# Optimization experiments

Measured on AMD Instinct MI355X. Metric: run time of the kernel, lower is better.

## Reference

```python
import jax, jax.numpy as jnp
import numpy as np

B, L, ENC, DEC, ATT = 128, 196, 2048, 512, 512

def setup_inputs() -> dict:
    key = jax.random.key(0)
    ks = jax.random.split(key, 8)
    s_enc = 1.0 / np.sqrt(ENC)
    s_dec = 1.0 / np.sqrt(DEC)
    s_att = 1.0 / np.sqrt(ATT)
    return {
        "encoder_out": jax.random.normal(ks[0], (B, L, ENC), jnp.float32),
        "decoder_hidden": jax.random.normal(ks[1], (B, DEC), jnp.float32),
        "We": jax.random.uniform(ks[2], (ENC, ATT), jnp.float32, -s_enc, s_enc),
        "be": jax.random.uniform(ks[3], (ATT,), jnp.float32, -s_enc, s_enc),
        "Wd": jax.random.uniform(ks[4], (DEC, ATT), jnp.float32, -s_dec, s_dec),
        "bd": jax.random.uniform(ks[5], (ATT,), jnp.float32, -s_dec, s_dec),
        "wa": jax.random.uniform(ks[6], (ATT,), jnp.float32, -s_att, s_att),
        "ba": jax.random.uniform(ks[7], (), jnp.float32, -s_att, s_att),
    }

def reference(encoder_out, decoder_hidden, We, be, Wd, bd, wa, ba):
    # encoder_out: [B, L, ENC]; decoder_hidden: [B, DEC]
    enc_map = jnp.einsum('ble,ea->bla', encoder_out, We) + be          # [B, L, A]
    dec_map = decoder_hidden @ Wd + bd                                  # [B, A]
    scores = jnp.tanh(enc_map + dec_map[:, None, :]) @ wa + ba         # [B, L]
    alphas = jax.nn.softmax(scores, axis=1)                             # [B, L]
    context = jnp.einsum('bl,ble->be', alphas, encoder_out)             # [B, ENC]
    return (context, alphas)
```

## Files before the change

kernel.cpp:

```cpp
#include <hip/hip_runtime.h>

#define B_   128
#define L_   196
#define ENC_ 2048
#define DEC_ 512
#define ATT_ 512
#define M_   (B_ * L_)

typedef _Float16 f16x4 __attribute__((ext_vector_type(4)));
typedef _Float16 f16x8 __attribute__((ext_vector_type(8)));
typedef __fp16   h16x2 __attribute__((ext_vector_type(2)));
typedef float    f32x4 __attribute__((ext_vector_type(4)));

#define FENCE_LDS_BARRIER()                                        \
    do {                                                           \
        asm volatile("s_waitcnt lgkmcnt(0)" ::: "memory");         \
        __builtin_amdgcn_s_barrier();                              \
        __builtin_amdgcn_sched_barrier(0);                         \
    } while (0)


__global__ void wets_kernel(const float* __restrict__ We, _Float16* __restrict__ WeTs) {
    int u = blockIdx.x * 256 + threadIdx.x;
    int row = u & 127;
    int k8  = (u >> 7) & 3;
    int kt  = (u >> 9) & 63;
    int nt  = u >> 15;
    int n  = nt * 128 + row;
    int k0 = kt * 32 + k8 * 8;
    f16x8 h;
#pragma unroll
    for (int j = 0; j < 8; ++j) h[j] = (_Float16)We[(k0 + j) * ATT_ + n];
    *reinterpret_cast<f16x8*>(WeTs + (size_t)u * 8) = h;
}

__global__ void decmap_kernel(const float* __restrict__ dh, const float* __restrict__ Wd,
                              const float* __restrict__ bd, float* __restrict__ dec) {
    int b = blockIdx.x;
    int a = threadIdx.x;
    float acc = bd[a];
    const float* dhp = dh + b * DEC_;
#pragma unroll 8
    for (int k = 0; k < DEC_; ++k) acc += dhp[k] * Wd[k * ATT_ + a];
    dec[b * ATT_ + a] = acc;
}

__global__ __launch_bounds__(256, 3)
void gemm_score_kernel(const float* __restrict__ enc,
                       const _Float16* __restrict__ WeTs,
                       const float* __restrict__ be,
                       const float* __restrict__ wa,
                       const float* __restrict__ dec,
                       float* __restrict__ partial) {
    __shared__ _Float16 smem[3][4096];
    __shared__ float red[2][128];

    int bid = blockIdx.x;
    int sid = (bid & 7) * 98 + (bid >> 3);
    int mtile = sid >> 2;
    int ntile = sid & 3;

    int tid  = threadIdx.x;
    int lane = tid & 63, wid = tid >> 6;
    int wm = wid >> 1, wn = wid & 1;
    int l15 = lane & 15, lg = lane >> 4;

    int arowi = tid >> 2;
    int ac8   = tid & 3;
    const float* agA = enc + (size_t)(mtile * 128 + arowi) * ENC_ + ac8 * 8;
    const float* agB = agA + (size_t)64 * ENC_;
    int wa0 = (ac8 * 128 + (arowi ^ (2 * ac8))) * 8;
    int wa1 = wa0 + 64 * 8;

    const _Float16* bfr = WeTs +
        ((size_t)ntile * 64 * 4 * 128 + (size_t)lg * 128 + wn * 64 + l15) * 8;

    int afo = (lg * 128 + wm * 64 + (l15 ^ (2 * lg))) * 8;

    float4 areg0[4], areg1[4], areg2[4];
    f16x8  bf0[4], bf1[4];

    f32x4 acc[4][4];
#pragma unroll
    for (int mi = 0; mi < 4; ++mi)
#pragma unroll
        for (int ni = 0; ni < 4; ++ni) acc[mi][ni] = (f32x4){0.f, 0.f, 0.f, 0.f};

#define DEF_LOADA(S)                                                     \
    auto loadA##S = [&](int kt) {                                        \
        const float* a0 = agA + kt * 32;                                 \
        const float* a1 = agB + kt * 32;                                 \
        areg##S[0] = *reinterpret_cast<const float4*>(a0);               \
        areg##S[1] = *reinterpret_cast<const float4*>(a0 + 4);           \
        areg##S[2] = *reinterpret_cast<const float4*>(a1);               \
        areg##S[3] = *reinterpret_cast<const float4*>(a1 + 4);           \
    }
    DEF_LOADA(0); DEF_LOADA(1); DEF_LOADA(2);
#undef DEF_LOADA

#define DEF_LOADB(S)                                                     \
    auto loadB##S = [&](int kt) {                                        \
        const _Float16* s = bfr + (size_t)kt * 4096;                     \
        bf##S[0] = *reinterpret_cast<const f16x8*>(s + 0 * 128);         \
        bf##S[1] = *reinterpret_cast<const f16x8*>(s + 16 * 8);          \
        bf##S[2] = *reinterpret_cast<const f16x8*>(s + 32 * 8);         \
        bf##S[3] = *reinterpret_cast<const f16x8*>(s + 48 * 8);          \
    }
    DEF_LOADB(0); DEF_LOADB(1);
#undef DEF_LOADB

#define DEF_WRITEA(S)                                                    \
    auto writeA##S = [&](int buf) {                                      \
        _Float16* As = smem[buf];                                        \
        union { h16x2 h2[4]; f16x8 h8; } cv;                             \
        cv.h2[0] = __builtin_amdgcn_cvt_pkrtz(areg##S[0].x, areg##S[0].y); \
        cv.h2[1] = __builtin_amdgcn_cvt_pkrtz(areg##S[0].z, areg##S[0].w); \
        cv.h2[2] = __builtin_amdgcn_cvt_pkrtz(areg##S[1].x, areg##S[1].y); \
        cv.h2[3] = __builtin_amdgcn_cvt_pkrtz(areg##S[1].z, areg##S[1].w); \
        *reinterpret_cast<f16x8*>(As + wa0) = cv.h8;                     \
        cv.h2[0] = __builtin_amdgcn_cvt_pkrtz(areg##S[2].x, areg##S[2].y); \
        cv.h2[1] = __builtin_amdgcn_cvt_pkrtz(areg##S[2].z, areg##S[2].w); \
        cv.h2[2] = __builtin_amdgcn_cvt_pkrtz(areg##S[3].x, areg##S[3].y); \
        cv.h2[3] = __builtin_amdgcn_cvt_pkrtz(areg##S[3].z, areg##S[3].w); \
        *reinterpret_cast<f16x8*>(As + wa1) = cv.h8;                     \
    }
    DEF_WRITEA(0); DEF_WRITEA(1); DEF_WRITEA(2);
#undef DEF_WRITEA

    auto compute = [&](const _Float16* As, const f16x8* bf) {
        f16x8 af[4];
#pragma unroll
        for (int mi = 0; mi < 4; ++mi)
            af[mi] = *reinterpret_cast<const f16x8*>(As + afo + mi * 128);
        __builtin_amdgcn_s_setprio(1);
#pragma unroll
        for (int mi = 0; mi < 4; ++mi)
#pragma unroll
            for (int ni = 0; ni < 4; ++ni)
                acc[mi][ni] = __builtin_amdgcn_mfma_f32_16x16x32_f16(
                    af[mi], bf[ni], acc[mi][ni], 0, 0, 0);
        __builtin_amdgcn_s_setprio(0);
    };

#define PHASE(KT, S, WS, BS, CBS, RBUF, WBUF)                            \
    do {                                                                 \
        int ka = (KT) + 3 < 64 ? (KT) + 3 : 63;                          \
        int kb = (KT) + 1 < 64 ? (KT) + 1 : 63;                          \
        loadB##BS(kb);                                                   \
        __builtin_amdgcn_sched_barrier(0);                               \
        loadA##S(ka);                                                    \
        writeA##WS(WBUF);                                                \
        FENCE_LDS_BARRIER();                                             \
        compute(smem[RBUF], bf##CBS);                                    \
    } while (0)

    loadB0(0);
    __builtin_amdgcn_sched_barrier(0);
    loadA0(0);
    loadA1(1);
    loadA2(2);
    writeA0(0);
    FENCE_LDS_BARRIER();

    for (int kt6 = 0; kt6 < 10; ++kt6) {
        int kt = kt6 * 6;
        PHASE(kt + 0, 0, 1, 1, 0, 0, 1);
        PHASE(kt + 1, 1, 2, 0, 1, 1, 2);
        PHASE(kt + 2, 2, 0, 1, 0, 2, 0);
        PHASE(kt + 3, 0, 1, 0, 1, 0, 1);
        PHASE(kt + 4, 1, 2, 1, 0, 1, 2);
        PHASE(kt + 5, 2, 0, 0, 1, 2, 0);
    }
    PHASE(60, 0, 1, 1, 0, 0, 1);
    PHASE(61, 1, 2, 0, 1, 1, 2);
    PHASE(62, 2, 0, 1, 0, 2, 0);
    PHASE(63, 0, 1, 0, 1, 0, 1);
#undef PHASE

    float rsum[4][4];
#pragma unroll
    for (int mi = 0; mi < 4; ++mi)
#pragma unroll
        for (int j = 0; j < 4; ++j) rsum[mi][j] = 0.f;

    int nb = ntile * 128 + wn * 64;
    int rb = mtile * 128 + wm * 64;
#pragma unroll
    for (int ni = 0; ni < 4; ++ni) {
        int n = nb + ni * 16 + l15;
        float wav = wa[n];
        float bev = be[n];
#pragma unroll
        for (int mi = 0; mi < 4; ++mi) {
#pragma unroll
            for (int j = 0; j < 4; ++j) {
                int row = rb + mi * 16 + lg * 4 + j;
                int b = row / L_;
                float x = acc[mi][ni][j] + bev + dec[b * ATT_ + n];
                float e = __expf(2.0f * x);
                float t = 1.0f - 2.0f / (e + 1.0f);
                rsum[mi][j] += t * wav;
            }
        }
    }
#pragma unroll
    for (int mi = 0; mi < 4; ++mi) {
#pragma unroll
        for (int j = 0; j < 4; ++j) {
            float v = rsum[mi][j];
            v += __shfl_xor(v, 1);
            v += __shfl_xor(v, 2);
            v += __shfl_xor(v, 4);
            v += __shfl_xor(v, 8);
            if (l15 == 0) red[wn][wm * 64 + mi * 16 + lg * 4 + j] = v;
        }
    }
    __syncthreads();
    if (tid < 128)
        partial[(size_t)ntile * M_ + mtile * 128 + tid] = red[0][tid] + red[1][tid];
}

__global__ void softmax_kernel(const float* __restrict__ partial, float* __restrict__ alphas) {
    int b = blockIdx.x, t = threadIdx.x;
    int lane = t & 63, wid = t >> 6;
    __shared__ float red[4];
    float s = 0.f, val = -1e30f;
    if (t < L_) {
        int r = b * L_ + t;
        s = partial[r] + partial[M_ + r] + partial[2 * M_ + r] + partial[3 * M_ + r];
        val = s;
    }
    float m = val;
#pragma unroll
    for (int off = 1; off < 64; off <<= 1) m = fmaxf(m, __shfl_xor(m, off));
    if (lane == 0) red[wid] = m;
    __syncthreads();
    m = fmaxf(fmaxf(red[0], red[1]), fmaxf(red[2], red[3]));
    float e = (t < L_) ? __expf(s - m) : 0.f;
    float sum = e;
#pragma unroll
    for (int off = 1; off < 64; off <<= 1) sum += __shfl_xor(sum, off);
    __syncthreads();
    if (lane == 0) red[wid] = sum;
    __syncthreads();
    sum = red[0] + red[1] + red[2] + red[3];
    if (t < L_) alphas[b * L_ + t] = e / sum;
}

__global__ void context_kernel(const float* __restrict__ enc, const float* __restrict__ alphas,
                               float* __restrict__ ctx) {
    int b = blockIdx.x >> 2;
    int ec = blockIdx.x & 3;
    int e = ec * 512 + threadIdx.x * 2;
    const float* ep = enc + (size_t)b * L_ * ENC_ + e;
    const float* ap = alphas + b * L_;
    float ax = 0.f, ay = 0.f;
#pragma unroll 4
    for (int l = 0; l < L_; ++l) {
        float a = ap[l];
        float2 v = *reinterpret_cast<const float2*>(ep + (size_t)l * ENC_);
        ax += a * v.x;
        ay += a * v.y;
    }
    float2 r; r.x = ax; r.y = ay;
    *reinterpret_cast<float2*>(&ctx[b * ENC_ + e]) = r;
}

extern "C" void kernel_launch(void* const* d_in, const int* in_sizes, int n_in,
                              void* d_out, int out_size, void* d_ws, size_t ws_size,
                              hipStream_t stream) {
    const float* enc = (const float*)d_in[0];
    const float* dh  = (const float*)d_in[1];
    const float* We  = (const float*)d_in[2];
    const float* be  = (const float*)d_in[3];
    const float* Wd  = (const float*)d_in[4];
    const float* bd  = (const float*)d_in[5];
    const float* wa  = (const float*)d_in[6];

    float* out    = (float*)d_out;
    float* ctx    = out;
    float* alphas = out + B_ * ENC_;

    char* ws = (char*)d_ws;
    float*    dec     = (float*)ws;
    _Float16* WeTs    = (_Float16*)(ws + 262144);
    float*    partial = (float*)(ws + 262144 + 2097152);

    hipLaunchKernelGGL(wets_kernel,       dim3(512),  dim3(256), 0, stream, We, WeTs);
    hipLaunchKernelGGL(decmap_kernel,     dim3(128),  dim3(512), 0, stream, dh, Wd, bd, dec);
    hipLaunchKernelGGL(gemm_score_kernel, dim3(784),  dim3(256), 0, stream, enc, WeTs, be, wa, dec, partial);
    hipLaunchKernelGGL(softmax_kernel,    dim3(128),  dim3(256), 0, stream, partial, alphas);
    hipLaunchKernelGGL(context_kernel,    dim3(512),  dim3(256), 0, stream, enc, alphas, ctx);
}
```

Baseline: 165.9 us.

## Compute full attention width per block to avoid re-reading encoder rows

```diff
diff --git a/kernel.cpp b/kernel.cpp
--- a/kernel.cpp
+++ b/kernel.cpp
@@ -45,55 +45,46 @@
     dec[b * ATT_ + a] = acc;
 }
 
-__global__ __launch_bounds__(256, 3)
+__global__ __launch_bounds__(512, 1)
 void gemm_score_kernel(const float* __restrict__ enc,
                        const _Float16* __restrict__ WeTs,
                        const float* __restrict__ be,
                        const float* __restrict__ wa,
                        const float* __restrict__ dec,
-                       float* __restrict__ partial) {
+                       float* __restrict__ scores) {
     __shared__ _Float16 smem[3][4096];
-    __shared__ float red[2][128];
-
-    int bid = blockIdx.x;
-    int sid = (bid & 7) * 98 + (bid >> 3);
-    int mtile = sid >> 2;
-    int ntile = sid & 3;
-
+    __shared__ float red[4][128];
+
+    int mtile = blockIdx.x;
     int tid  = threadIdx.x;
     int lane = tid & 63, wid = tid >> 6;
-    int wm = wid >> 1, wn = wid & 1;
+    int wm = wid >> 2, wn = wid & 3;
     int l15 = lane & 15, lg = lane >> 4;
 
     int arowi = tid >> 2;
     int ac8   = tid & 3;
-    const float* agA = enc + (size_t)(mtile * 128 + arowi) * ENC_ + ac8 * 8;
-    const float* agB = agA + (size_t)64 * ENC_;
+    const float* ag = enc + (size_t)(mtile * 128 + arowi) * ENC_ + ac8 * 8;
     int wa0 = (ac8 * 128 + (arowi ^ (2 * ac8))) * 8;
-    int wa1 = wa0 + 64 * 8;
 
     const _Float16* bfr = WeTs +
-        ((size_t)ntile * 64 * 4 * 128 + (size_t)lg * 128 + wn * 64 + l15) * 8;
+        ((size_t)wn * 64 * 4 * 128 + (size_t)lg * 128 + l15) * 8;
 
     int afo = (lg * 128 + wm * 64 + (l15 ^ (2 * lg))) * 8;
 
-    float4 areg0[4], areg1[4], areg2[4];
-    f16x8  bf0[4], bf1[4];
-
-    f32x4 acc[4][4];
+    float4 areg0[2], areg1[2], areg2[2];
+    f16x8  bf0[8], bf1[8];
+
+    f32x4 acc[4][8];
 #pragma unroll
     for (int mi = 0; mi < 4; ++mi)
 #pragma unroll
-        for (int ni = 0; ni < 4; ++ni) acc[mi][ni] = (f32x4){0.f, 0.f, 0.f, 0.f};
+        for (int ni = 0; ni < 8; ++ni) acc[mi][ni] = (f32x4){0.f, 0.f, 0.f, 0.f};
 
 #define DEF_LOADA(S)                                                     \
     auto loadA##S = [&](int kt) {                                        \
-        const float* a0 = agA + kt * 32;                                 \
-        const float* a1 = agB + kt * 32;                                 \
+        const float* a0 = ag + kt * 32;                                  \
         areg##S[0] = *reinterpret_cast<const float4*>(a0);               \
         areg##S[1] = *reinterpret_cast<const float4*>(a0 + 4);           \
-        areg##S[2] = *reinterpret_cast<const float4*>(a1);               \
-        areg##S[3] = *reinterpret_cast<const float4*>(a1 + 4);           \
     }
     DEF_LOADA(0); DEF_LOADA(1); DEF_LOADA(2);
 #undef DEF_LOADA
@@ -102,9 +93,13 @@
     auto loadB##S = [&](int kt) {                                        \
         const _Float16* s = bfr + (size_t)kt * 4096;                     \
         bf##S[0] = *reinterpret_cast<const f16x8*>(s + 0 * 128);         \
-        bf##S[1] = *reinterpret_cast<const f16x8*>(s + 16 * 8);          \
-        bf##S[2] = *reinterpret_cast<const f16x8*>(s + 32 * 8);         \
-        bf##S[3] = *reinterpret_cast<const f16x8*>(s + 48 * 8);          \
+        bf##S[1] = *reinterpret_cast<const f16x8*>(s + 1 * 128);         \
+        bf##S[2] = *reinterpret_cast<const f16x8*>(s + 2 * 128);         \
+        bf##S[3] = *reinterpret_cast<const f16x8*>(s + 3 * 128);         \
+        bf##S[4] = *reinterpret_cast<const f16x8*>(s + 4 * 128);         \
+        bf##S[5] = *reinterpret_cast<const f16x8*>(s + 5 * 128);         \
+        bf##S[6] = *reinterpret_cast<const f16x8*>(s + 6 * 128);         \
+        bf##S[7] = *reinterpret_cast<const f16x8*>(s + 7 * 128);         \
     }
     DEF_LOADB(0); DEF_LOADB(1);
 #undef DEF_LOADB
@@ -118,11 +113,6 @@
         cv.h2[2] = __builtin_amdgcn_cvt_pkrtz(areg##S[1].x, areg##S[1].y); \
         cv.h2[3] = __builtin_amdgcn_cvt_pkrtz(areg##S[1].z, areg##S[1].w); \
         *reinterpret_cast<f16x8*>(As + wa0) = cv.h8;                     \
-        cv.h2[0] = __builtin_amdgcn_cvt_pkrtz(areg##S[2].x, areg##S[2].y); \
-        cv.h2[1] = __builtin_amdgcn_cvt_pkrtz(areg##S[2].z, areg##S[2].w); \
-        cv.h2[2] = __builtin_amdgcn_cvt_pkrtz(areg##S[3].x, areg##S[3].y); \
-        cv.h2[3] = __builtin_amdgcn_cvt_pkrtz(areg##S[3].z, areg##S[3].w); \
-        *reinterpret_cast<f16x8*>(As + wa1) = cv.h8;                     \
     }
     DEF_WRITEA(0); DEF_WRITEA(1); DEF_WRITEA(2);
 #undef DEF_WRITEA
@@ -136,7 +126,7 @@
 #pragma unroll
         for (int mi = 0; mi < 4; ++mi)
 #pragma unroll
-            for (int ni = 0; ni < 4; ++ni)
+            for (int ni = 0; ni < 8; ++ni)
                 acc[mi][ni] = __builtin_amdgcn_mfma_f32_16x16x32_f16(
                     af[mi], bf[ni], acc[mi][ni], 0, 0, 0);
         __builtin_amdgcn_s_setprio(0);
@@ -183,11 +173,10 @@
 #pragma unroll
         for (int j = 0; j < 4; ++j) rsum[mi][j] = 0.f;
 
-    int nb = ntile * 128 + wn * 64;
     int rb = mtile * 128 + wm * 64;
 #pragma unroll
-    for (int ni = 0; ni < 4; ++ni) {
-        int n = nb + ni * 16 + l15;
+    for (int ni = 0; ni < 8; ++ni) {
+        int n = wn * 128 + ni * 16 + l15;
         float wav = wa[n];
         float bev = be[n];
 #pragma unroll
@@ -217,17 +206,16 @@
     }
     __syncthreads();
     if (tid < 128)
-        partial[(size_t)ntile * M_ + mtile * 128 + tid] = red[0][tid] + red[1][tid];
-}
-
-__global__ void softmax_kernel(const float* __restrict__ partial, float* __restrict__ alphas) {
+        scores[mtile * 128 + tid] = red[0][tid] + red[1][tid] + red[2][tid] + red[3][tid];
+}
+
+__global__ void softmax_kernel(const float* __restrict__ scores, float* __restrict__ alphas) {
     int b = blockIdx.x, t = threadIdx.x;
     int lane = t & 63, wid = t >> 6;
     __shared__ float red[4];
     float s = 0.f, val = -1e30f;
     if (t < L_) {
-        int r = b * L_ + t;
-        s = partial[r] + partial[M_ + r] + partial[2 * M_ + r] + partial[3 * M_ + r];
+        s = scores[b * L_ + t];
         val = s;
     }
     float m = val;
@@ -284,11 +272,11 @@
     char* ws = (char*)d_ws;
     float*    dec     = (float*)ws;
     _Float16* WeTs    = (_Float16*)(ws + 262144);
-    float*    partial = (float*)(ws + 262144 + 2097152);
+    float*    scores  = (float*)(ws + 262144 + 2097152);
 
     hipLaunchKernelGGL(wets_kernel,       dim3(512),  dim3(256), 0, stream, We, WeTs);
     hipLaunchKernelGGL(decmap_kernel,     dim3(128),  dim3(512), 0, stream, dh, Wd, bd, dec);
-    hipLaunchKernelGGL(gemm_score_kernel, dim3(784),  dim3(256), 0, stream, enc, WeTs, be, wa, dec, partial);
-    hipLaunchKernelGGL(softmax_kernel,    dim3(128),  dim3(256), 0, stream, partial, alphas);
+    hipLaunchKernelGGL(gemm_score_kernel, dim3(196),  dim3(512), 0, stream, enc, WeTs, be, wa, dec, scores);
+    hipLaunchKernelGGL(softmax_kernel,    dim3(128),  dim3(256), 0, stream, scores, alphas);
     hipLaunchKernelGGL(context_kernel,    dim3(512),  dim3(256), 0, stream, enc, alphas, ctx);
 }
```

Measured after the change: 143.2 us. 13.6% less time.

## Halve GEMM M-tile and stream B tiles into LDS via global_load_lds

Applied to the files above, without the earlier changes.

```diff
diff --git a/kernel.cpp b/kernel.cpp
--- a/kernel.cpp
+++ b/kernel.cpp
@@ -7,7 +7,6 @@
 #define ATT_ 512
 #define M_   (B_ * L_)
 
-typedef _Float16 f16x4 __attribute__((ext_vector_type(4)));
 typedef _Float16 f16x8 __attribute__((ext_vector_type(8)));
 typedef __fp16   h16x2 __attribute__((ext_vector_type(2)));
 typedef float    f32x4 __attribute__((ext_vector_type(4)));
@@ -18,6 +17,12 @@
         __builtin_amdgcn_s_barrier();                              \
         __builtin_amdgcn_sched_barrier(0);                         \
     } while (0)
+
+__device__ __forceinline__ void gload16(const _Float16* g, _Float16* l) {
+    __builtin_amdgcn_global_load_lds(
+        (const __attribute__((address_space(1))) void*)g,
+        (__attribute__((address_space(3))) void*)l, 16, 0, 0);
+}
 
 
 __global__ void wets_kernel(const float* __restrict__ We, _Float16* __restrict__ WeTs) {
@@ -45,40 +50,39 @@
     dec[b * ATT_ + a] = acc;
 }
 
-__global__ __launch_bounds__(256, 3)
+__global__ __launch_bounds__(128, 3)
 void gemm_score_kernel(const float* __restrict__ enc,
                        const _Float16* __restrict__ WeTs,
                        const float* __restrict__ be,
                        const float* __restrict__ wa,
                        const float* __restrict__ dec,
                        float* __restrict__ partial) {
-    __shared__ _Float16 smem[3][4096];
-    __shared__ float red[2][128];
+    __shared__ _Float16 As[2][2048];
+    __shared__ _Float16 Bs[2][4096];
+    __shared__ float red[2][64];
 
     int bid = blockIdx.x;
-    int sid = (bid & 7) * 98 + (bid >> 3);
+    int sid = (bid & 7) * 196 + (bid >> 3);
     int mtile = sid >> 2;
     int ntile = sid & 3;
 
     int tid  = threadIdx.x;
-    int lane = tid & 63, wid = tid >> 6;
-    int wm = wid >> 1, wn = wid & 1;
+    int lane = tid & 63;
+    int wn   = tid >> 6;
     int l15 = lane & 15, lg = lane >> 4;
 
-    int arowi = tid >> 2;
-    int ac8   = tid & 3;
-    const float* agA = enc + (size_t)(mtile * 128 + arowi) * ENC_ + ac8 * 8;
-    const float* agB = agA + (size_t)64 * ENC_;
-    int wa0 = (ac8 * 128 + (arowi ^ (2 * ac8))) * 8;
-    int wa1 = wa0 + 64 * 8;
-
-    const _Float16* bfr = WeTs +
-        ((size_t)ntile * 64 * 4 * 128 + (size_t)lg * 128 + wn * 64 + l15) * 8;
-
-    int afo = (lg * 128 + wm * 64 + (l15 ^ (2 * lg))) * 8;
-
-    float4 areg0[4], areg1[4], areg2[4];
-    f16x8  bf0[4], bf1[4];
+    int arow = tid >> 1;
+    int h    = tid & 1;
+    const float* ag = enc + (size_t)(mtile * 64 + arow) * ENC_ + h * 16;
+    int wa0 = ((2 * h) * 64 + (arow ^ (4 * h))) * 8;
+    int wa1 = ((2 * h + 1) * 64 + (arow ^ (4 * h + 2))) * 8;
+
+    const _Float16* bsrc = WeTs + (size_t)ntile * 64 * 4096;
+
+    int afo = (lg * 64 + (l15 ^ (2 * lg))) * 8;
+    int bfo = (lg * 128 + wn * 64 + l15) * 8;
+
+    float4 areg0[4], areg1[4];
 
     f32x4 acc[4][4];
 #pragma unroll
@@ -88,94 +92,97 @@
 
 #define DEF_LOADA(S)                                                     \
     auto loadA##S = [&](int kt) {                                        \
-        const float* a0 = agA + kt * 32;                                 \
-        const float* a1 = agB + kt * 32;                                 \
-        areg##S[0] = *reinterpret_cast<const float4*>(a0);               \
-        areg##S[1] = *reinterpret_cast<const float4*>(a0 + 4);           \
-        areg##S[2] = *reinterpret_cast<const float4*>(a1);               \
-        areg##S[3] = *reinterpret_cast<const float4*>(a1 + 4);           \
-    }
-    DEF_LOADA(0); DEF_LOADA(1); DEF_LOADA(2);
+        const float* a = ag + kt * 32;                                   \
+        areg##S[0] = *reinterpret_cast<const float4*>(a);                \
+        areg##S[1] = *reinterpret_cast<const float4*>(a + 4);            \
+        areg##S[2] = *reinterpret_cast<const float4*>(a + 8);            \
+        areg##S[3] = *reinterpret_cast<const float4*>(a + 12);           \
+    }
+    DEF_LOADA(0); DEF_LOADA(1);
 #undef DEF_LOADA
-
-#define DEF_LOADB(S)                                                     \
-    auto loadB##S = [&](int kt) {                                        \
-        const _Float16* s = bfr + (size_t)kt * 4096;                     \
-        bf##S[0] = *reinterpret_cast<const f16x8*>(s + 0 * 128);         \
-        bf##S[1] = *reinterpret_cast<const f16x8*>(s + 16 * 8);          \
-        bf##S[2] = *reinterpret_cast<const f16x8*>(s + 32 * 8);         \
-        bf##S[3] = *reinterpret_cast<const f16x8*>(s + 48 * 8);          \
-    }
-    DEF_LOADB(0); DEF_LOADB(1);
-#undef DEF_LOADB
 
 #define DEF_WRITEA(S)                                                    \
     auto writeA##S = [&](int buf) {                                      \
-        _Float16* As = smem[buf];                                        \
+        _Float16* Ap = As[buf];                                          \
         union { h16x2 h2[4]; f16x8 h8; } cv;                             \
         cv.h2[0] = __builtin_amdgcn_cvt_pkrtz(areg##S[0].x, areg##S[0].y); \
         cv.h2[1] = __builtin_amdgcn_cvt_pkrtz(areg##S[0].z, areg##S[0].w); \
         cv.h2[2] = __builtin_amdgcn_cvt_pkrtz(areg##S[1].x, areg##S[1].y); \
         cv.h2[3] = __builtin_amdgcn_cvt_pkrtz(areg##S[1].z, areg##S[1].w); \
-        *reinterpret_cast<f16x8*>(As + wa0) = cv.h8;                     \
+        *reinterpret_cast<f16x8*>(Ap + wa0) = cv.h8;                     \
         cv.h2[0] = __builtin_amdgcn_cvt_pkrtz(areg##S[2].x, areg##S[2].y); \
         cv.h2[1] = __builtin_amdgcn_cvt_pkrtz(areg##S[2].z, areg##S[2].w); \
         cv.h2[2] = __builtin_amdgcn_cvt_pkrtz(areg##S[3].x, areg##S[3].y); \
         cv.h2[3] = __builtin_amdgcn_cvt_pkrtz(areg##S[3].z, areg##S[3].w); \
-        *reinterpret_cast<f16x8*>(As + wa1) = cv.h8;                     \
-    }
-    DEF_WRITEA(0); DEF_WRITEA(1); DEF_WRITEA(2);
+        *reinterpret_cast<f16x8*>(Ap + wa1) = cv.h8;                     \
+    }
+    DEF_WRITEA(0); DEF_WRITEA(1);
 #undef DEF_WRITEA
 
-    auto compute = [&](const _Float16* As, const f16x8* bf) {
-        f16x8 af[4];
+    auto dmab = [&](int buf, int kt) {
+        const _Float16* s = bsrc + (size_t)kt * 4096;
+#pragma unroll
+        for (int j = 0; j < 4; ++j)
+            gload16(s + (j * 128 + tid) * 8, &Bs[buf][(j * 128 + tid) * 8]);
+    };
+    auto compute = [&](int buf) {
+        const _Float16* Ap = As[buf];
+        const _Float16* Bp = Bs[buf];
+        f16x8 af[4], bf[4];
 #pragma unroll
         for (int mi = 0; mi < 4; ++mi)
-            af[mi] = *reinterpret_cast<const f16x8*>(As + afo + mi * 128);
-        __builtin_amdgcn_s_setprio(1);
+            af[mi] = *reinterpret_cast<const f16x8*>(Ap + afo + mi * 128);
+#pragma unroll
+        for (int ni = 0; ni < 4; ++ni)
+            bf[ni] = *reinterpret_cast<const f16x8*>(Bp + bfo + ni * 128);
 #pragma unroll
         for (int mi = 0; mi < 4; ++mi)
 #pragma unroll
             for (int ni = 0; ni < 4; ++ni)
                 acc[mi][ni] = __builtin_amdgcn_mfma_f32_16x16x32_f16(
                     af[mi], bf[ni], acc[mi][ni], 0, 0, 0);
-        __builtin_amdgcn_s_setprio(0);
     };
 
-#define PHASE(KT, S, WS, BS, CBS, RBUF, WBUF)                            \
-    do {                                                                 \
-        int ka = (KT) + 3 < 64 ? (KT) + 3 : 63;                          \
-        int kb = (KT) + 1 < 64 ? (KT) + 1 : 63;                          \
-        loadB##BS(kb);                                                   \
-        __builtin_amdgcn_sched_barrier(0);                               \
-        loadA##S(ka);                                                    \
-        writeA##WS(WBUF);                                                \
-        FENCE_LDS_BARRIER();                                             \
-        compute(smem[RBUF], bf##CBS);                                    \
-    } while (0)
-
-    loadB0(0);
+    dmab(0, 0);
     __builtin_amdgcn_sched_barrier(0);
     loadA0(0);
     loadA1(1);
-    loadA2(2);
     writeA0(0);
+    asm volatile("s_waitcnt vmcnt(4)" ::: "memory");
+    __builtin_amdgcn_sched_barrier(0);
     FENCE_LDS_BARRIER();
 
-    for (int kt6 = 0; kt6 < 10; ++kt6) {
-        int kt = kt6 * 6;
-        PHASE(kt + 0, 0, 1, 1, 0, 0, 1);
-        PHASE(kt + 1, 1, 2, 0, 1, 1, 2);
-        PHASE(kt + 2, 2, 0, 1, 0, 2, 0);
-        PHASE(kt + 3, 0, 1, 0, 1, 0, 1);
-        PHASE(kt + 4, 1, 2, 1, 0, 1, 2);
-        PHASE(kt + 5, 2, 0, 0, 1, 2, 0);
-    }
-    PHASE(60, 0, 1, 1, 0, 0, 1);
-    PHASE(61, 1, 2, 0, 1, 1, 2);
-    PHASE(62, 2, 0, 1, 0, 2, 0);
-    PHASE(63, 0, 1, 0, 1, 0, 1);
-#undef PHASE
+    for (int k2 = 0; k2 < 32; ++k2) {
+        int k = k2 * 2;
+        {
+            int kb = k + 1;
+            int ka = k + 2 < 64 ? k + 2 : 63;
+            dmab(1, kb);
+            __builtin_amdgcn_sched_barrier(0);
+            loadA0(ka);
+            __builtin_amdgcn_sched_barrier(0);
+            compute(0);
+            __builtin_amdgcn_sched_barrier(0);
+            writeA1(1);
+            asm volatile("s_waitcnt vmcnt(4)" ::: "memory");
+            __builtin_amdgcn_sched_barrier(0);
+            FENCE_LDS_BARRIER();
+        }
+        {
+            int kb = k + 2 < 64 ? k + 2 : 63;
+            int ka = k + 3 < 64 ? k + 3 : 63;
+            dmab(0, kb);
+            __builtin_amdgcn_sched_barrier(0);
+            loadA1(ka);
+            __builtin_amdgcn_sched_barrier(0);
+            compute(1);
+            __builtin_amdgcn_sched_barrier(0);
+            writeA0(0);
+            asm volatile("s_waitcnt vmcnt(4)" ::: "memory");
+            __builtin_amdgcn_sched_barrier(0);
+            FENCE_LDS_BARRIER();
+        }
+    }
 
     float rsum[4][4];
 #pragma unroll
@@ -183,11 +190,10 @@
 #pragma unroll
         for (int j = 0; j < 4; ++j) rsum[mi][j] = 0.f;
 
-    int nb = ntile * 128 + wn * 64;
-    int rb = mtile * 128 + wm * 64;
+    int rb = mtile * 64;
 #pragma unroll
     for (int ni = 0; ni < 4; ++ni) {
-        int n = nb + ni * 16 + l15;
+        int n = ntile * 128 + wn * 64 + ni * 16 + l15;
         float wav = wa[n];
         float bev = be[n];
 #pragma unroll
@@ -212,12 +218,12 @@
             v += __shfl_xor(v, 2);
             v += __shfl_xor(v, 4);
             v += __shfl_xor(v, 8);
-            if (l15 == 0) red[wn][wm * 64 + mi * 16 + lg * 4 + j] = v;
+            if (l15 == 0) red[wn][mi * 16 + lg * 4 + j] = v;
         }
     }
     __syncthreads();
-    if (tid < 128)
-        partial[(size_t)ntile * M_ + mtile * 128 + tid] = red[0][tid] + red[1][tid];
+    if (tid < 64)
+        partial[(size_t)ntile * M_ + mtile * 64 + tid] = red[0][tid] + red[1][tid];
 }
 
 __global__ void softmax_kernel(const float* __restrict__ partial, float* __restrict__ alphas) {
@@ -284,11 +290,11 @@
     char* ws = (char*)d_ws;
     float*    dec     = (float*)ws;
     _Float16* WeTs    = (_Float16*)(ws + 262144);
-    float*    partial = (float*)(ws + 262144 + 2097152);
+    float*    partial = (float*)(ws + 2359296);
 
     hipLaunchKernelGGL(wets_kernel,       dim3(512),  dim3(256), 0, stream, We, WeTs);
     hipLaunchKernelGGL(decmap_kernel,     dim3(128),  dim3(512), 0, stream, dh, Wd, bd, dec);
-    hipLaunchKernelGGL(gemm_score_kernel, dim3(784),  dim3(256), 0, stream, enc, WeTs, be, wa, dec, partial);
+    hipLaunchKernelGGL(gemm_score_kernel, dim3(1568), dim3(128), 0, stream, enc, WeTs, be, wa, dec, partial);
     hipLaunchKernelGGL(softmax_kernel,    dim3(128),  dim3(256), 0, stream, partial, alphas);
     hipLaunchKernelGGL(context_kernel,    dim3(512),  dim3(256), 0, stream, enc, alphas, ctx);
 }
```

Result: slower. 190.4 us (+14.8%).
